# Performance work log

Measured on AMD Instinct MI355X. Metric: run time of the kernel, lower is better.

The kernel has to match this reference:

```python
import jax, jax.numpy as jnp
import numpy as np
from jax import lax

MOMENTUM = 0.2  # from init_kwargs
NUM_SAMPLES = 50000
NUM_FEATURES = 1024
BATCH = 8192


def setup_inputs() -> dict:
    key = jax.random.key(0)
    k1, k2, k3 = jax.random.split(key, 3)
    f_out = jax.random.normal(k1, (BATCH, NUM_FEATURES), dtype=jnp.float32)
    features = jax.random.normal(k2, (NUM_SAMPLES, NUM_FEATURES), dtype=jnp.float32)
    p_labels = jax.random.randint(k3, (BATCH,), 0, NUM_SAMPLES, dtype=jnp.int64)
    return {"f_out": f_out, "features": features, "p_labels": p_labels}


def reference(f_out, features, p_labels):
    # Faithful sequential semantics of the Python for-loop in update():
    # duplicate labels must see the previously-updated (and normalized) row,
    # so we use lax.scan (recurrence over the batch) rather than a parallel scatter.
    m = jnp.float32(MOMENTUM)

    def step(bank, xy):
        x, y = xy  # x: [F], y: scalar int
        old = bank[y]                      # gather row [F]
        v = m * old + (1.0 - m) * x        # momentum blend
        v = v / jnp.linalg.norm(v)         # L2 normalize (matches .norm())
        bank = bank.at[y].set(v)           # scatter write
        return bank, None

    updated, _ = lax.scan(step, features, (f_out, p_labels))
    return updated
```

## Files before the change

kernel.cpp:

```cpp
#include <hip/hip_runtime.h>

#define BATCH 8192
#define NF 1024
#define NS 50000
#define MOM 0.2f
#define MAXOCC 64

__global__ void build_firstlast(const int* __restrict__ labels,
                                int* __restrict__ first,
                                int* __restrict__ lastm) {
    const int i = blockIdx.x * blockDim.x + threadIdx.x;
    if (i >= BATCH) return;
    const int y = labels[i];
    atomicMin(&first[y], i);
    atomicMin(&lastm[y], BATCH - 1 - i);
}

__device__ __forceinline__ void blend_normalize(float4& v, const float4 x,
                                                float* s_part, int tid) {
    const float m = MOM, om = 1.0f - MOM;
    v.x = m * v.x + om * x.x;
    v.y = m * v.y + om * x.y;
    v.z = m * v.z + om * x.z;
    v.w = m * v.w + om * x.w;
    float s = v.x * v.x + v.y * v.y + v.z * v.z + v.w * v.w;
    for (int off = 32; off; off >>= 1) s += __shfl_xor(s, off, 64);
    if ((tid & 63) == 0) s_part[tid >> 6] = s;
    __syncthreads();
    const float tot = s_part[0] + s_part[1] + s_part[2] + s_part[3];
    __syncthreads();
    const float inv = 1.0f / sqrtf(tot);
    v.x *= inv; v.y *= inv; v.z *= inv; v.w *= inv;
}

__global__ __launch_bounds__(256)
void fused_bank(const float* __restrict__ f_out,
                const float* __restrict__ features,
                const int* __restrict__ labels,
                const int* __restrict__ first,
                const int* __restrict__ lastm,
                float* __restrict__ out) {
    const int y = blockIdx.x;
    const int tid = threadIdx.x;
    const float4* feat4 = reinterpret_cast<const float4*>(features);
    const float4* fout4 = reinterpret_cast<const float4*>(f_out);

    float4 v = feat4[(size_t)y * (NF / 4) + tid];

    const int h = first[y];
    if (h < BATCH) {
        __shared__ float s_part[4];
        const int l = BATCH - 1 - lastm[y];
        if (h == l) {
            blend_normalize(v, fout4[(size_t)h * (NF / 4) + tid], s_part, tid);
        } else {
            __shared__ int s_cnt;
            __shared__ int s_idx[MAXOCC];
            if (tid == 0) s_cnt = 0;
            __syncthreads();
            for (int j = tid; j < BATCH; j += 256) {
                if (labels[j] == y) {
                    const int p = atomicAdd(&s_cnt, 1);
                    if (p < MAXOCC) s_idx[p] = j;
                }
            }
            __syncthreads();
            const int n = min(s_cnt, MAXOCC);
            if (tid == 0) {
                for (int a = 1; a < n; ++a) {
                    const int key = s_idx[a];
                    int b = a - 1;
                    while (b >= 0 && s_idx[b] > key) { s_idx[b + 1] = s_idx[b]; --b; }
                    s_idx[b + 1] = key;
                }
            }
            __syncthreads();
            for (int t = 0; t < n; ++t)
                blend_normalize(v, fout4[(size_t)s_idx[t] * (NF / 4) + tid],
                                s_part, tid);
        }
    }
    reinterpret_cast<float4*>(out)[(size_t)y * (NF / 4) + tid] = v;
}

extern "C" void kernel_launch(void* const* d_in, const int* in_sizes, int n_in,
                              void* d_out, int out_size, void* d_ws, size_t ws_size,
                              hipStream_t stream) {
    const float* f_out    = (const float*)d_in[0];
    const float* features = (const float*)d_in[1];
    const int*   labels   = (const int*)d_in[2];
    float* out = (float*)d_out;

    int* first = (int*)d_ws;
    int* lastm = first + NS;

    hipMemsetAsync(first, 0x7F, (size_t)2 * NS * sizeof(int), stream);
    build_firstlast<<<(BATCH + 255) / 256, 256, 0, stream>>>(labels, first, lastm);
    fused_bank<<<NS, 256, 0, stream>>>(f_out, features, labels, first, lastm, out);
}
```

Baseline: 94.70 us.

## Merge table init into cooperative prelude and persist bank kernel with row prefetch

Replaces the memset plus first/last build kernel with a single cooperative kernel that initializes the table, does a grid sync, then runs the atomics. This saves one launch. The main bank kernel now uses 2048 persistent blocks that stride over the rows, software-prefetching the next two feature rows and their first/last entries into registers while the current row is processed. The aim is to hide memory latency and cut block-launch overhead, at the cost of more registers and fewer resident waves to hide latency.

```diff
diff --git a/kernel.cpp b/kernel.cpp
--- a/kernel.cpp
+++ b/kernel.cpp
@@ -1,19 +1,26 @@
 #include <hip/hip_runtime.h>
+#include <hip/hip_cooperative_groups.h>
+
+namespace cg = cooperative_groups;
 
 #define BATCH 8192
 #define NF 1024
 #define NS 50000
 #define MOM 0.2f
 #define MAXOCC 64
+#define GBLK 2048
+#define PRE_BLKS 256
 
-__global__ void build_firstlast(const int* __restrict__ labels,
-                                int* __restrict__ first,
-                                int* __restrict__ lastm) {
-    const int i = blockIdx.x * blockDim.x + threadIdx.x;
-    if (i >= BATCH) return;
-    const int y = labels[i];
-    atomicMin(&first[y], i);
-    atomicMin(&lastm[y], BATCH - 1 - i);
+__global__ __launch_bounds__(256)
+void prelude(const int* __restrict__ labels, int* __restrict__ table) {
+    const int idx = blockIdx.x * 256 + threadIdx.x;
+    for (int t = idx; t < 2 * NS; t += PRE_BLKS * 256) table[t] = 0x7f7f7f7f;
+    cg::this_grid().sync();
+    if (idx < BATCH) {
+        const int y = labels[idx];
+        atomicMin(&table[y], idx);
+        atomicMin(&table[NS + y], BATCH - 1 - idx);
+    }
 }
 
 __device__ __forceinline__ void blend_normalize(float4& v, const float4 x,
@@ -40,47 +47,73 @@
                 const int* __restrict__ first,
                 const int* __restrict__ lastm,
                 float* __restrict__ out) {
-    const int y = blockIdx.x;
     const int tid = threadIdx.x;
+    const int bid = blockIdx.x;
     const float4* feat4 = reinterpret_cast<const float4*>(features);
     const float4* fout4 = reinterpret_cast<const float4*>(f_out);
+    float4* out4 = reinterpret_cast<float4*>(out);
 
-    float4 v = feat4[(size_t)y * (NF / 4) + tid];
+    __shared__ float s_part[4];
+    __shared__ int s_cnt;
+    __shared__ int s_idx[MAXOCC];
 
-    const int h = first[y];
-    if (h < BATCH) {
-        __shared__ float s_part[4];
-        const int l = BATCH - 1 - lastm[y];
-        if (h == l) {
-            blend_normalize(v, fout4[(size_t)h * (NF / 4) + tid], s_part, tid);
-        } else {
-            __shared__ int s_cnt;
-            __shared__ int s_idx[MAXOCC];
-            if (tid == 0) s_cnt = 0;
-            __syncthreads();
-            for (int j = tid; j < BATCH; j += 256) {
-                if (labels[j] == y) {
-                    const int p = atomicAdd(&s_cnt, 1);
-                    if (p < MAXOCC) s_idx[p] = j;
+    int y0 = bid;
+    int y1 = y0 + GBLK;
+    float4 v0{}, v1{};
+    int h0 = 0, l0 = 0, h1 = 0, l1 = 0;
+    if (y0 < NS) {
+        v0 = feat4[(size_t)y0 * (NF / 4) + tid];
+        h0 = first[y0];  l0 = lastm[y0];
+    }
+    if (y1 < NS) {
+        v1 = feat4[(size_t)y1 * (NF / 4) + tid];
+        h1 = first[y1];  l1 = lastm[y1];
+    }
+
+    while (y0 < NS) {
+        const int y2 = y1 + GBLK;
+        float4 v2{};
+        int h2 = 0, l2 = 0;
+        if (y2 < NS) {
+            v2 = feat4[(size_t)y2 * (NF / 4) + tid];
+            h2 = first[y2];  l2 = lastm[y2];
+        }
+
+        if (h0 < BATCH) {
+            const int last = BATCH - 1 - l0;
+            if (h0 == last) {
+                blend_normalize(v0, fout4[(size_t)h0 * (NF / 4) + tid], s_part, tid);
+            } else {
+                if (tid == 0) s_cnt = 0;
+                __syncthreads();
+                const int y = y0;
+                for (int j = tid; j < BATCH; j += 256) {
+                    if (labels[j] == y) {
+                        const int p = atomicAdd(&s_cnt, 1);
+                        if (p < MAXOCC) s_idx[p] = j;
+                    }
                 }
+                __syncthreads();
+                const int n = min(s_cnt, MAXOCC);
+                if (tid == 0) {
+                    for (int a = 1; a < n; ++a) {
+                        const int key = s_idx[a];
+                        int b = a - 1;
+                        while (b >= 0 && s_idx[b] > key) { s_idx[b + 1] = s_idx[b]; --b; }
+                        s_idx[b + 1] = key;
+                    }
+                }
+                __syncthreads();
+                for (int t = 0; t < n; ++t)
+                    blend_normalize(v0, fout4[(size_t)s_idx[t] * (NF / 4) + tid],
+                                    s_part, tid);
             }
-            __syncthreads();
-            const int n = min(s_cnt, MAXOCC);
-            if (tid == 0) {
-                for (int a = 1; a < n; ++a) {
-                    const int key = s_idx[a];
-                    int b = a - 1;
-                    while (b >= 0 && s_idx[b] > key) { s_idx[b + 1] = s_idx[b]; --b; }
-                    s_idx[b + 1] = key;
-                }
-            }
-            __syncthreads();
-            for (int t = 0; t < n; ++t)
-                blend_normalize(v, fout4[(size_t)s_idx[t] * (NF / 4) + tid],
-                                s_part, tid);
         }
+        out4[(size_t)y0 * (NF / 4) + tid] = v0;
+
+        y0 = y1; v0 = v1; h0 = h1; l0 = l1;
+        y1 = y2; v1 = v2; h1 = h2; l1 = l2;
     }
-    reinterpret_cast<float4*>(out)[(size_t)y * (NF / 4) + tid] = v;
 }
 
 extern "C" void kernel_launch(void* const* d_in, const int* in_sizes, int n_in,
@@ -91,10 +124,13 @@
     const int*   labels   = (const int*)d_in[2];
     float* out = (float*)d_out;
 
-    int* first = (int*)d_ws;
-    int* lastm = first + NS;
+    int* table = (int*)d_ws;
+    int* first = table;
+    int* lastm = table + NS;
 
-    hipMemsetAsync(first, 0x7F, (size_t)2 * NS * sizeof(int), stream);
-    build_firstlast<<<(BATCH + 255) / 256, 256, 0, stream>>>(labels, first, lastm);
-    fused_bank<<<NS, 256, 0, stream>>>(f_out, features, labels, first, lastm, out);
+    void* pre_args[] = { (void*)&labels, (void*)&table };
+    hipLaunchCooperativeKernel(reinterpret_cast<void*>(prelude),
+                               dim3(PRE_BLKS), dim3(256), pre_args, 0, stream);
+
+    fused_bank<<<GBLK, 256, 0, stream>>>(f_out, features, labels, first, lastm, out);
 }
```

After: 146.1 us. 1.54x slower.

## Self-resetting label table, one-wave blocks, and nontemporal vector loads/stores

Applied to the files above, without the earlier changes.

Removes the per-call hipMemsetAsync. Each touched entry of the packed first/last table is reset to a sentinel inside the kernel, and a labels[h]==y check guards against stale or garbage workspace contents. The main kernel now uses 64-thread single-wavefront blocks with four float4 chunks per lane, so the norm reduction needs only a wave shuffle and no shared memory or __syncthreads. Row loads and stores use nontemporal hints to avoid polluting the cache. The trade-off is reliance on workspace state persisting across calls, and a slower duplicate-label scan path when the workspace holds garbage.

```diff
diff --git a/kernel.cpp b/kernel.cpp
--- a/kernel.cpp
+++ b/kernel.cpp
@@ -5,60 +5,71 @@
 #define NS 50000
 #define MOM 0.2f
 #define MAXOCC 64
+#define SENT 0xAAAAAAAAu
+
+typedef float floatx4 __attribute__((ext_vector_type(4)));
 
 __global__ void build_firstlast(const int* __restrict__ labels,
-                                int* __restrict__ first,
-                                int* __restrict__ lastm) {
+                                uint2* __restrict__ table) {
     const int i = blockIdx.x * blockDim.x + threadIdx.x;
     if (i >= BATCH) return;
     const int y = labels[i];
-    atomicMin(&first[y], i);
-    atomicMin(&lastm[y], BATCH - 1 - i);
+    atomicMin(&table[y].x, (unsigned)i);
+    atomicMin(&table[y].y, (unsigned)(BATCH - 1 - i));
 }
 
-__device__ __forceinline__ void blend_normalize(float4& v, const float4 x,
-                                                float* s_part, int tid) {
+__device__ __forceinline__ void blend_normalize(floatx4& v0, floatx4& v1,
+                                                floatx4& v2, floatx4& v3,
+                                                const floatx4* __restrict__ xrow,
+                                                int tid) {
     const float m = MOM, om = 1.0f - MOM;
-    v.x = m * v.x + om * x.x;
-    v.y = m * v.y + om * x.y;
-    v.z = m * v.z + om * x.z;
-    v.w = m * v.w + om * x.w;
-    float s = v.x * v.x + v.y * v.y + v.z * v.z + v.w * v.w;
+    const floatx4 x0 = __builtin_nontemporal_load(&xrow[tid]);
+    const floatx4 x1 = __builtin_nontemporal_load(&xrow[tid + 64]);
+    const floatx4 x2 = __builtin_nontemporal_load(&xrow[tid + 128]);
+    const floatx4 x3 = __builtin_nontemporal_load(&xrow[tid + 192]);
+    v0 = m * v0 + om * x0;
+    v1 = m * v1 + om * x1;
+    v2 = m * v2 + om * x2;
+    v3 = m * v3 + om * x3;
+    float s = v0.x * v0.x + v0.y * v0.y + v0.z * v0.z + v0.w * v0.w
+            + v1.x * v1.x + v1.y * v1.y + v1.z * v1.z + v1.w * v1.w
+            + v2.x * v2.x + v2.y * v2.y + v2.z * v2.z + v2.w * v2.w
+            + v3.x * v3.x + v3.y * v3.y + v3.z * v3.z + v3.w * v3.w;
     for (int off = 32; off; off >>= 1) s += __shfl_xor(s, off, 64);
-    if ((tid & 63) == 0) s_part[tid >> 6] = s;
-    __syncthreads();
-    const float tot = s_part[0] + s_part[1] + s_part[2] + s_part[3];
-    __syncthreads();
-    const float inv = 1.0f / sqrtf(tot);
-    v.x *= inv; v.y *= inv; v.z *= inv; v.w *= inv;
+    const float inv = 1.0f / sqrtf(s);
+    v0 *= inv; v1 *= inv; v2 *= inv; v3 *= inv;
 }
 
-__global__ __launch_bounds__(256)
+__global__ __launch_bounds__(64)
 void fused_bank(const float* __restrict__ f_out,
                 const float* __restrict__ features,
                 const int* __restrict__ labels,
-                const int* __restrict__ first,
-                const int* __restrict__ lastm,
+                uint2* __restrict__ table,
                 float* __restrict__ out) {
     const int y = blockIdx.x;
     const int tid = threadIdx.x;
-    const float4* feat4 = reinterpret_cast<const float4*>(features);
-    const float4* fout4 = reinterpret_cast<const float4*>(f_out);
+    const floatx4* feat4 =
+        reinterpret_cast<const floatx4*>(features) + (size_t)y * (NF / 4);
+    const floatx4* fout4 = reinterpret_cast<const floatx4*>(f_out);
+    floatx4* out4 = reinterpret_cast<floatx4*>(out) + (size_t)y * (NF / 4);
 
-    float4 v = feat4[(size_t)y * (NF / 4) + tid];
+    floatx4 v0 = __builtin_nontemporal_load(&feat4[tid]);
+    floatx4 v1 = __builtin_nontemporal_load(&feat4[tid + 64]);
+    floatx4 v2 = __builtin_nontemporal_load(&feat4[tid + 128]);
+    floatx4 v3 = __builtin_nontemporal_load(&feat4[tid + 192]);
 
-    const int h = first[y];
+    const uint2 fl = table[y];
+    const unsigned h = fl.x;
     if (h < BATCH) {
-        __shared__ float s_part[4];
-        const int l = BATCH - 1 - lastm[y];
-        if (h == l) {
-            blend_normalize(v, fout4[(size_t)h * (NF / 4) + tid], s_part, tid);
+        const unsigned last = BATCH - 1u - fl.y;
+        if (h == last && labels[h] == y) {
+            blend_normalize(v0, v1, v2, v3, fout4 + (size_t)h * (NF / 4), tid);
         } else {
             __shared__ int s_cnt;
             __shared__ int s_idx[MAXOCC];
             if (tid == 0) s_cnt = 0;
             __syncthreads();
-            for (int j = tid; j < BATCH; j += 256) {
+            for (int j = tid; j < BATCH; j += 64) {
                 if (labels[j] == y) {
                     const int p = atomicAdd(&s_cnt, 1);
                     if (p < MAXOCC) s_idx[p] = j;
@@ -76,11 +87,16 @@
             }
             __syncthreads();
             for (int t = 0; t < n; ++t)
-                blend_normalize(v, fout4[(size_t)s_idx[t] * (NF / 4) + tid],
-                                s_part, tid);
+                blend_normalize(v0, v1, v2, v3,
+                                fout4 + (size_t)s_idx[t] * (NF / 4), tid);
         }
+        if (tid == 0) table[y] = make_uint2(SENT, SENT);
     }
-    reinterpret_cast<float4*>(out)[(size_t)y * (NF / 4) + tid] = v;
+
+    __builtin_nontemporal_store(v0, &out4[tid]);
+    __builtin_nontemporal_store(v1, &out4[tid + 64]);
+    __builtin_nontemporal_store(v2, &out4[tid + 128]);
+    __builtin_nontemporal_store(v3, &out4[tid + 192]);
 }
 
 extern "C" void kernel_launch(void* const* d_in, const int* in_sizes, int n_in,
@@ -91,10 +107,8 @@
     const int*   labels   = (const int*)d_in[2];
     float* out = (float*)d_out;
 
-    int* first = (int*)d_ws;
-    int* lastm = first + NS;
+    uint2* table = (uint2*)d_ws;
 
-    hipMemsetAsync(first, 0x7F, (size_t)2 * NS * sizeof(int), stream);
-    build_firstlast<<<(BATCH + 255) / 256, 256, 0, stream>>>(labels, first, lastm);
-    fused_bank<<<NS, 256, 0, stream>>>(f_out, features, labels, first, lastm, out);
+    build_firstlast<<<(BATCH + 255) / 256, 256, 0, stream>>>(labels, table);
+    fused_bank<<<NS, 64, 0, stream>>>(f_out, features, labels, table, out);
 }
```

After: 100.1 us. 1.06x slower.
